# Optimization experiments

Hardware: AMD Instinct MI355X
Metric: run time of the kernel (lower is better)

Reference implementation:

```python
import jax, jax.numpy as jnp
import numpy as np

D = 256; DFFN = 1024; H = 8; NLVL = 4; NPNT = 4; HD = D // H
BS = 4; NQ = 100; NPTS = 25
SPATIAL = [(128, 128), (64, 64), (32, 32), (16, 16)]
LEN_IN = sum(h * w for h, w in SPATIAL)


def _ln(x, g, b, eps=1e-5):
    m = x.mean(-1, keepdims=True)
    v = ((x - m) ** 2).mean(-1, keepdims=True)
    return (x - m) * jax.lax.rsqrt(v + eps) * g + b


def _mha(q, k, v, w_in, b_in, w_out, b_out):
    # torch nn.MultiheadAttention math, batch-first layout [B,S,D]
    B, Sq, _ = q.shape; Sk = k.shape[1]
    wq, wk, wv = jnp.split(w_in, 3, 0); bq, bk, bv = jnp.split(b_in, 3)
    qh = (q @ wq.T + bq).reshape(B, Sq, H, HD).transpose(0, 2, 1, 3)
    kh = (k @ wk.T + bk).reshape(B, Sk, H, HD).transpose(0, 2, 1, 3)
    vh = (v @ wv.T + bv).reshape(B, Sk, H, HD).transpose(0, 2, 1, 3)
    a = jax.nn.softmax(jnp.einsum('bhqd,bhkd->bhqk', qh, kh) * (1.0 / float(np.sqrt(HD))), -1)
    o = jnp.einsum('bhqk,bhkd->bhqd', a, vh).transpose(0, 2, 1, 3).reshape(B, Sq, D)
    return o @ w_out.T + b_out


def _msdeform(query, ref, src, off_w, off_b, aw_w, aw_b, val_w, val_b, out_w, out_b):
    # MSDeformAttn: per-query multi-level bilinear sampling + weighted aggregation
    bs, Lq, _ = query.shape
    value = (src @ val_w.T + val_b).reshape(bs, LEN_IN, H, HD)
    off = (query @ off_w.T + off_b).reshape(bs, Lq, H, NLVL, NPNT, 2)
    aw = jax.nn.softmax((query @ aw_w.T + aw_b).reshape(bs, Lq, H, NLVL * NPNT), -1)
    aw = aw.reshape(bs, Lq, H, NLVL, NPNT)
    norm = jnp.array([[w, h] for h, w in SPATIAL], jnp.float32)  # (W,H) per level
    loc = ref[:, :, None, :, None, :] + off / norm[None, None, None, :, None, :]
    out = jnp.zeros((bs, H, Lq, HD), query.dtype)
    start = 0
    for l, (hh, ww) in enumerate(SPATIAL):
        v_l = value[:, start:start + hh * ww].transpose(0, 2, 1, 3)  # [bs,H,hw,HD]
        start += hh * ww
        # grid_sample align_corners=False pixel coords: loc*size - 0.5
        x = (loc[:, :, :, l, :, 0] * ww - 0.5).transpose(0, 2, 1, 3).reshape(bs, H, Lq * NPNT)
        y = (loc[:, :, :, l, :, 1] * hh - 0.5).transpose(0, 2, 1, 3).reshape(bs, H, Lq * NPNT)
        x0 = jnp.floor(x); y0 = jnp.floor(y); wx = x - x0; wy = y - y0
        x0i = x0.astype(jnp.int32); y0i = y0.astype(jnp.int32); x1i = x0i + 1; y1i = y0i + 1
        def g(xi, yi):
            valid = ((xi >= 0) & (xi < ww) & (yi >= 0) & (yi < hh)).astype(query.dtype)
            idx = jnp.clip(yi, 0, hh - 1) * ww + jnp.clip(xi, 0, ww - 1)
            return jnp.take_along_axis(v_l, idx[..., None], axis=2) * valid[..., None]
        s = (g(x0i, y0i) * ((1 - wx) * (1 - wy))[..., None]
             + g(x1i, y0i) * (wx * (1 - wy))[..., None]
             + g(x0i, y1i) * ((1 - wx) * wy)[..., None]
             + g(x1i, y1i) * (wx * wy)[..., None])
        s = s.reshape(bs, H, Lq, NPNT, HD)
        out = out + (s * aw[:, :, :, l].transpose(0, 2, 1, 3)[..., None]).sum(3)
    return out.transpose(0, 2, 1, 3).reshape(bs, Lq, D) @ out_w.T + out_b


def _fwd(tgt, query_pos, reference_points, src,
         w_in_intra, b_in_intra, w_out_intra, b_out_intra, g_norm_intra, b_norm_intra,
         w_in_inter, b_in_inter, w_out_inter, b_out_inter, g_norm_inter, b_norm_inter,
         off_w, off_b, aw_w, aw_b, val_w, val_b, co_w, co_b, g_norm_cross, b_norm_cross,
         lin1_w, lin1_b, lin2_w, lin2_b, g_norm3, b_norm3):
    bs, nq, npts, d = tgt.shape
    # intra-instance self-attention (over control points)
    q = (tgt + query_pos).reshape(bs * nq, npts, d)
    t2 = _mha(q, q, tgt.reshape(bs * nq, npts, d), w_in_intra, b_in_intra, w_out_intra, b_out_intra)
    tgt = _ln(tgt + t2.reshape(bs, nq, npts, d), g_norm_intra, b_norm_intra)
    # inter-instance self-attention (over queries), no pos embed per source code
    ti = tgt.transpose(0, 2, 1, 3).reshape(bs * npts, nq, d)
    t2 = _mha(ti, ti, ti, w_in_inter, b_in_inter, w_out_inter, b_out_inter)
    ti = _ln(ti + t2, g_norm_inter, b_norm_inter).reshape(bs, npts, nq, d).transpose(0, 2, 1, 3)
    # deformable cross-attention
    ref = jnp.broadcast_to(reference_points[:, :, None], (bs, nq, npts, NLVL, 2)).reshape(bs, nq * npts, NLVL, 2)
    qc = (ti + query_pos).reshape(bs, nq * npts, d)
    t2 = _msdeform(qc, ref, src, off_w, off_b, aw_w, aw_b, val_w, val_b, co_w, co_b).reshape(bs, nq, npts, d)
    tgt = _ln(ti + t2, g_norm_cross, b_norm_cross)
    # FFN
    ff = jax.nn.relu(tgt @ lin1_w.T + lin1_b) @ lin2_w.T + lin2_b
    return _ln(tgt + ff, g_norm3, b_norm3)


def setup_inputs() -> dict:
    key = jax.random.key(0)
    ki = iter(jax.random.split(key, 40))
    def rn(shape, sc=0.02):
        return jax.random.normal(next(ki), shape, jnp.float32) * sc
    inp = dict(
        tgt=jax.random.normal(next(ki), (BS, NQ, NPTS, D), jnp.float32),
        query_pos=jax.random.normal(next(ki), (BS, NQ, NPTS, D), jnp.float32),
        reference_points=jax.random.uniform(next(ki), (BS, NQ, NLVL, 2), jnp.float32),
        src=jax.random.normal(next(ki), (BS, LEN_IN, D), jnp.float32),
        w_in_intra=rn((3 * D, D)), b_in_intra=jnp.zeros((3 * D,), jnp.float32),
        w_out_intra=rn((D, D)), b_out_intra=jnp.zeros((D,), jnp.float32),
        g_norm_intra=jnp.ones((D,), jnp.float32), b_norm_intra=jnp.zeros((D,), jnp.float32),
        w_in_inter=rn((3 * D, D)), b_in_inter=jnp.zeros((3 * D,), jnp.float32),
        w_out_inter=rn((D, D)), b_out_inter=jnp.zeros((D,), jnp.float32),
        g_norm_inter=jnp.ones((D,), jnp.float32), b_norm_inter=jnp.zeros((D,), jnp.float32),
        off_w=rn((H * NLVL * NPNT * 2, D), 0.001), off_b=rn((H * NLVL * NPNT * 2,), 0.5),
        aw_w=rn((H * NLVL * NPNT, D)), aw_b=jnp.zeros((H * NLVL * NPNT,), jnp.float32),
        val_w=rn((D, D)), val_b=jnp.zeros((D,), jnp.float32),
        co_w=rn((D, D)), co_b=jnp.zeros((D,), jnp.float32),
        g_norm_cross=jnp.ones((D,), jnp.float32), b_norm_cross=jnp.zeros((D,), jnp.float32),
        lin1_w=rn((DFFN, D)), lin1_b=jnp.zeros((DFFN,), jnp.float32),
        lin2_w=rn((D, DFFN)), lin2_b=jnp.zeros((D,), jnp.float32),
        g_norm3=jnp.ones((D,), jnp.float32), b_norm3=jnp.zeros((D,), jnp.float32),
        src_spatial_shapes=jnp.array(SPATIAL, jnp.int32),
        level_start_index=jnp.array(np.cumsum([0] + [h * w for h, w in SPATIAL[:-1]]), jnp.int32),
    )
    return inp


def reference(tgt, query_pos, reference_points, src,
              w_in_intra, b_in_intra, w_out_intra, b_out_intra, g_norm_intra, b_norm_intra,
              w_in_inter, b_in_inter, w_out_inter, b_out_inter, g_norm_inter, b_norm_inter,
              off_w, off_b, aw_w, aw_b, val_w, val_b, co_w, co_b, g_norm_cross, b_norm_cross,
              lin1_w, lin1_b, lin2_w, lin2_b, g_norm3, b_norm3,
              src_spatial_shapes, level_start_index):
    # spatial shapes / level starts are compile-time constants (SPATIAL); args kept for signature parity
    return _fwd(tgt, query_pos, reference_points, src,
                w_in_intra, b_in_intra, w_out_intra, b_out_intra, g_norm_intra, b_norm_intra,
                w_in_inter, b_in_inter, w_out_inter, b_out_inter, g_norm_inter, b_norm_inter,
                off_w, off_b, aw_w, aw_b, val_w, val_b, co_w, co_b, g_norm_cross, b_norm_cross,
                lin1_w, lin1_b, lin2_w, lin2_b, g_norm3, b_norm3)
```

## Files before the change

### kernel.cpp

```cpp
#include <hip/hip_runtime.h>
#include <math.h>

#define DMODEL 256
#define HEADS  8
#define HDIM   32
#define BS     4
#define NQ     100
#define NPTS   25
#define LQ     2500
#define M10K   10000
#define LEN_IN 21760
#define MVAL   87040

typedef float f32x4 __attribute__((ext_vector_type(4)));
typedef short s16x8 __attribute__((ext_vector_type(8)));
typedef unsigned short u16;

static __device__ __forceinline__ short f2bf(float f) {
    unsigned u = __builtin_bit_cast(unsigned, f);
    u = (u + 0x7fffu + ((u >> 16) & 1u)) >> 16;
    return (short)u;
}
static __device__ __forceinline__ unsigned pack2(float lo, float hi) {
    return (unsigned)(u16)f2bf(lo) | ((unsigned)(u16)f2bf(hi) << 16);
}
static __device__ __forceinline__ float bf_lo(unsigned u) {
    return __builtin_bit_cast(float, u << 16);
}
static __device__ __forceinline__ float bf_hi(unsigned u) {
    return __builtin_bit_cast(float, u & 0xffff0000u);
}

#define LDSK   40
#define LDSK64 72

__global__ __launch_bounds__(256) void fat_stage0_kernel(
    const float* __restrict__ s0, const float* __restrict__ s1,
    const float* __restrict__ s2, const float* __restrict__ s3,
    const float* __restrict__ s4, const float* __restrict__ s5,
    const float* __restrict__ s6, const float* __restrict__ s7,
    const float* __restrict__ s8, const float* __restrict__ s9,
    u16* __restrict__ dst,
    const float* __restrict__ a, const float* __restrict__ b,
    u16* __restrict__ xb, u16* __restrict__ ab)
{
    if (blockIdx.x < 624) {
        int t8 = (blockIdx.x * 256 + threadIdx.x) * 8;
        if (t8 >= 1277952) return;
        const float* s; int base;
        if      (t8 <  196608) { s = s0; base = 0;       }
        else if (t8 <  262144) { s = s1; base = 196608;  }
        else if (t8 <  458752) { s = s2; base = 262144;  }
        else if (t8 <  524288) { s = s3; base = 458752;  }
        else if (t8 <  589824) { s = s4; base = 524288;  }
        else if (t8 <  622592) { s = s5; base = 589824;  }
        else if (t8 <  688128) { s = s6; base = 622592;  }
        else if (t8 <  753664) { s = s7; base = 688128;  }
        else if (t8 < 1015808) { s = s8; base = 753664;  }
        else                   { s = s9; base = 1015808; }
        const float* p = s + (t8 - base);
        float4 fa = *(const float4*)p;
        float4 fb = *(const float4*)(p + 4);
        s16x8 v;
        v[0]=f2bf(fa.x); v[1]=f2bf(fa.y); v[2]=f2bf(fa.z); v[3]=f2bf(fa.w);
        v[4]=f2bf(fb.x); v[5]=f2bf(fb.y); v[6]=f2bf(fb.z); v[7]=f2bf(fb.w);
        *(s16x8*)(dst + t8) = v;
    } else {
        int i = (blockIdx.x - 624) * 256 + threadIdx.x;
        size_t o = (size_t)i * 8;
        float4 a0 = *(const float4*)(a + o);
        float4 a1 = *(const float4*)(a + o + 4);
        s16x8 v;
        v[0]=f2bf(a0.x); v[1]=f2bf(a0.y); v[2]=f2bf(a0.z); v[3]=f2bf(a0.w);
        v[4]=f2bf(a1.x); v[5]=f2bf(a1.y); v[6]=f2bf(a1.z); v[7]=f2bf(a1.w);
        *(s16x8*)(ab + o) = v;
        float4 b0 = *(const float4*)(b + o);
        float4 b1 = *(const float4*)(b + o + 4);
        a0.x += b0.x; a0.y += b0.y; a0.z += b0.z; a0.w += b0.w;
        a1.x += b1.x; a1.y += b1.y; a1.z += b1.z; a1.w += b1.w;
        s16x8 w;
        w[0]=f2bf(a0.x); w[1]=f2bf(a0.y); w[2]=f2bf(a0.z); w[3]=f2bf(a0.w);
        w[4]=f2bf(a1.x); w[5]=f2bf(a1.y); w[6]=f2bf(a1.z); w[7]=f2bf(a1.w);
        *(s16x8*)(xb + o) = w;
    }
}


static __device__ __forceinline__ void body_value64(
    char* smem_, const float* __restrict__ A, const u16* __restrict__ W,
    const float* __restrict__ bias, u16* __restrict__ C, int bx, int by)
{
    short* As = (short*)smem_;
    short* Ws = (short*)(smem_ + 5120);

    const int tid = threadIdx.x;
    const int n0 = bx * 128;
    const int m0 = by * 64;

    const int arow = tid >> 2;
    const int ak = (tid & 3) * 8;
    const int wrow = tid >> 1;
    const int wk = (tid & 1) * 16;

    const float* aptr = A + (size_t)(m0 + arow) * 256 + ak;
    const u16* wptr = W + (size_t)(n0 + wrow) * 256 + wk;

    const int wave = tid >> 6;
    const int wm = wave & 1, wn = wave >> 1;
    const int lane = tid & 63;
    const int lrow = lane & 15, kq = lane >> 4;

    f32x4 acc[2][4];
#pragma unroll
    for (int i = 0; i < 2; ++i)
#pragma unroll
        for (int j = 0; j < 4; ++j) acc[i][j] = (f32x4)(0.f);

    float4 pa0 = *(const float4*)aptr;
    float4 pa1 = *(const float4*)(aptr + 4);
    s16x8 w0 = *(const s16x8*)wptr;
    s16x8 w1 = *(const s16x8*)(wptr + 8);

    for (int k0 = 0; k0 < 256; k0 += 32) {
        s16x8 av;
        av[0]=f2bf(pa0.x); av[1]=f2bf(pa0.y); av[2]=f2bf(pa0.z); av[3]=f2bf(pa0.w);
        av[4]=f2bf(pa1.x); av[5]=f2bf(pa1.y); av[6]=f2bf(pa1.z); av[7]=f2bf(pa1.w);
        *(s16x8*)&As[arow * LDSK + ak]     = av;
        *(s16x8*)&Ws[wrow * LDSK + wk]     = w0;
        *(s16x8*)&Ws[wrow * LDSK + wk + 8] = w1;
        __syncthreads();
        if (k0 + 32 < 256) {
            pa0 = *(const float4*)(aptr + k0 + 32);
            pa1 = *(const float4*)(aptr + k0 + 36);
            w0 = *(const s16x8*)(wptr + k0 + 32);
            w1 = *(const s16x8*)(wptr + k0 + 40);
        }

        s16x8 af[2], bfv[4];
#pragma unroll
        for (int i = 0; i < 2; ++i)
            af[i] = *(const s16x8*)&As[(wm * 32 + i * 16 + lrow) * LDSK + kq * 8];
#pragma unroll
        for (int j = 0; j < 4; ++j)
            bfv[j] = *(const s16x8*)&Ws[(wn * 64 + j * 16 + lrow) * LDSK + kq * 8];
#pragma unroll
        for (int i = 0; i < 2; ++i)
#pragma unroll
            for (int j = 0; j < 4; ++j)
                acc[i][j] = __builtin_amdgcn_mfma_f32_16x16x32_bf16(af[i], bfv[j], acc[i][j], 0, 0, 0);
        __syncthreads();
    }

#pragma unroll
    for (int i = 0; i < 2; ++i)
#pragma unroll
        for (int j = 0; j < 4; ++j) {
            int col = n0 + wn * 64 + j * 16 + lrow;
            float bv = bias[col];
#pragma unroll
            for (int reg = 0; reg < 4; ++reg) {
                int gmo = m0 + wm * 32 + i * 16 + kq * 4 + reg;
                C[(size_t)gmo * 256 + col] = (u16)f2bf(acc[i][j][reg] + bv);
            }
        }
}

static __device__ __forceinline__ void body_mfma128(
    char* smem_, const u16* __restrict__ A, const u16* __restrict__ W,
    const float* __restrict__ bias, u16* __restrict__ Cv, int bx, int by)
{
    short* As = (short*)smem_;
    short* Ws = (short*)(smem_ + 10240);

    const int tid = threadIdx.x;
    const int m0 = by * 128, n0 = bx * 128;
    const int srow = tid >> 1;
    const int sk = (tid & 1) * 16;
    const int wave = tid >> 6;
    const int wm = wave & 1, wn = wave >> 1;
    const int lane = tid & 63;
    const int lrow = lane & 15, kq = lane >> 4;

    const int gm = m0 + srow;
    const u16* aptr = A + (size_t)gm * 256 + sk;
    const u16* wptr = W + (size_t)(n0 + srow) * 256 + sk;

    f32x4 acc[4][4];
#pragma unroll
    for (int i = 0; i < 4; ++i)
#pragma unroll
        for (int j = 0; j < 4; ++j) acc[i][j] = (f32x4)(0.f);

    s16x8 a0 = (s16x8)0, a1 = (s16x8)0, w0, w1;
    if (gm < M10K) { a0 = *(const s16x8*)aptr; a1 = *(const s16x8*)(aptr + 8); }
    w0 = *(const s16x8*)wptr; w1 = *(const s16x8*)(wptr + 8);

    for (int k0 = 0; k0 < 256; k0 += 32) {
        *(s16x8*)&As[srow * LDSK + sk]     = a0;
        *(s16x8*)&As[srow * LDSK + sk + 8] = a1;
        *(s16x8*)&Ws[srow * LDSK + sk]     = w0;
        *(s16x8*)&Ws[srow * LDSK + sk + 8] = w1;
        __syncthreads();
        if (k0 + 32 < 256) {
            if (gm < M10K) {
                a0 = *(const s16x8*)(aptr + k0 + 32);
                a1 = *(const s16x8*)(aptr + k0 + 40);
            }
            w0 = *(const s16x8*)(wptr + k0 + 32);
            w1 = *(const s16x8*)(wptr + k0 + 40);
        }

        s16x8 af[4], bfv[4];
#pragma unroll
        for (int i = 0; i < 4; ++i)
            af[i] = *(const s16x8*)&As[(wm * 64 + i * 16 + lrow) * LDSK + kq * 8];
#pragma unroll
        for (int j = 0; j < 4; ++j)
            bfv[j] = *(const s16x8*)&Ws[(wn * 64 + j * 16 + lrow) * LDSK + kq * 8];
#pragma unroll
        for (int i = 0; i < 4; ++i)
#pragma unroll
            for (int j = 0; j < 4; ++j)
                acc[i][j] = __builtin_amdgcn_mfma_f32_16x16x32_bf16(af[i], bfv[j], acc[i][j], 0, 0, 0);
        __syncthreads();
    }

#pragma unroll
    for (int i = 0; i < 4; ++i)
#pragma unroll
        for (int j = 0; j < 4; ++j) {
            int col = n0 + wn * 64 + j * 16 + lrow;
            float bv = bias[col];
#pragma unroll
            for (int reg = 0; reg < 4; ++reg) {
                int gmo = m0 + wm * 64 + i * 16 + kq * 4 + reg;
                if (gmo < M10K)
                    Cv[(size_t)gmo * 768 + col] = (u16)f2bf(acc[i][j][reg] + bv);
            }
        }
}

static __device__ __forceinline__ void body_mfma64(
    char* smem_, const u16* __restrict__ A, const u16* __restrict__ W,
    const float* __restrict__ bias, u16* __restrict__ Cv, int bx, int by)
{
    short* As = (short*)smem_;
    short* Ws = (short*)(smem_ + 9216);

    const int tid = threadIdx.x;
    const int m0 = by * 64, n0 = bx * 64;
    const int srow = tid >> 2;
    const int sk = (tid & 3) * 16;
    const int wave = tid >> 6;
    const int wm = wave & 1, wn = wave >> 1;
    const int lane = tid & 63;
    const int lrow = lane & 15, kq = lane >> 4;

    const int gm = m0 + srow;
    const u16* aptr = A + (size_t)gm * 256 + sk;
    const u16* wptr = W + (size_t)(n0 + srow) * 256 + sk;

    f32x4 acc[2][2];
#pragma unroll
    for (int i = 0; i < 2; ++i)
#pragma unroll
        for (int j = 0; j < 2; ++j) acc[i][j] = (f32x4)(0.f);

    s16x8 a0 = (s16x8)0, a1 = (s16x8)0, w0, w1;
    if (gm < M10K) { a0 = *(const s16x8*)aptr; a1 = *(const s16x8*)(aptr + 8); }
    w0 = *(const s16x8*)wptr; w1 = *(const s16x8*)(wptr + 8);

    for (int k0 = 0; k0 < 256; k0 += 64) {
        *(s16x8*)&As[srow * LDSK64 + sk]     = a0;
        *(s16x8*)&As[srow * LDSK64 + sk + 8] = a1;
        *(s16x8*)&Ws[srow * LDSK64 + sk]     = w0;
        *(s16x8*)&Ws[srow * LDSK64 + sk + 8] = w1;
        __syncthreads();
        if (k0 + 64 < 256) {
            if (gm < M10K) {
                a0 = *(const s16x8*)(aptr + k0 + 64);
                a1 = *(const s16x8*)(aptr + k0 + 72);
            }
            w0 = *(const s16x8*)(wptr + k0 + 64);
            w1 = *(const s16x8*)(wptr + k0 + 72);
        }

#pragma unroll
        for (int s = 0; s < 2; ++s) {
            s16x8 af[2], bfv[2];
#pragma unroll
            for (int i = 0; i < 2; ++i)
                af[i] = *(const s16x8*)&As[(wm * 32 + i * 16 + lrow) * LDSK64 + s * 32 + kq * 8];
#pragma unroll
            for (int j = 0; j < 2; ++j)
                bfv[j] = *(const s16x8*)&Ws[(wn * 32 + j * 16 + lrow) * LDSK64 + s * 32 + kq * 8];
#pragma unroll
            for (int i = 0; i < 2; ++i)
#pragma unroll
                for (int j = 0; j < 2; ++j)
                    acc[i][j] = __builtin_amdgcn_mfma_f32_16x16x32_bf16(af[i], bfv[j], acc[i][j], 0, 0, 0);
        }
        __syncthreads();
    }

#pragma unroll
    for (int i = 0; i < 2; ++i)
#pragma unroll
        for (int j = 0; j < 2; ++j) {
            int col = n0 + wn * 32 + j * 16 + lrow;
            float bv = bias[col];
#pragma unroll
            for (int reg = 0; reg < 4; ++reg) {
                int gmo = m0 + wm * 32 + i * 16 + kq * 4 + reg;
                if (gmo < M10K)
                    Cv[(size_t)gmo * 768 + col] = (u16)f2bf(acc[i][j][reg] + bv);
            }
        }
}

__global__ __launch_bounds__(256) void fat_stage1_kernel(
    const float* __restrict__ src, const u16* __restrict__ wval,
    const float* __restrict__ valb, u16* __restrict__ valueb,
    const u16* __restrict__ x1b, const u16* __restrict__ wqk,
    const float* __restrict__ bqk, u16* __restrict__ qkvb,
    const u16* __restrict__ tgtb, const u16* __restrict__ wv,
    const float* __restrict__ bv, u16* __restrict__ qkvb_v)
{
    __shared__ __align__(16) char smem[20480];
    const int b = blockIdx.x;
    if (b < 2720) {
        body_value64(smem, src, wval, valb, valueb, b & 1, b >> 1);
    } else if (b < 3036) {
        const int bb = b - 2720;
        body_mfma128(smem, x1b, wqk, bqk, qkvb, bb & 3, bb >> 2);
    } else {
        const int bb = b - 3036;
        body_mfma64(smem, tgtb, wv, bv, qkvb_v, bb & 3, bb >> 2);
    }
}

__global__ __launch_bounds__(256) void gemm_mfma_kernel(
    const u16* __restrict__ A, int lda,
    const u16* __restrict__ W, int K,
    const float* __restrict__ bias,
    void* __restrict__ Cv, int ldc,
    int M, int relu, int out_bf16,
    int ncut, const float* __restrict__ bias2,
    float* __restrict__ Cv2, int ldc2)
{
    __shared__ short As[64 * LDSK64];
    __shared__ short Ws[64 * LDSK64];

    const int tid = threadIdx.x;
    const int m0 = blockIdx.y * 64, n0 = blockIdx.x * 64;
    const int srow = tid >> 2;
    const int sk = (tid & 3) * 16;
    const int wave = tid >> 6;
    const int wm = wave & 1, wn = wave >> 1;
    const int lane = tid & 63;
    const int lrow = lane & 15;
    const int kq = lane >> 4;

    const int gm = m0 + srow;
    const u16* aptr = A + (size_t)gm * lda + sk;
    const u16* wptr = W + (size_t)(n0 + srow) * K + sk;

    f32x4 acc[2][2];
#pragma unroll
    for (int i = 0; i < 2; ++i)
#pragma unroll
        for (int j = 0; j < 2; ++j) acc[i][j] = (f32x4)(0.f);

    s16x8 a0 = (s16x8)0, a1 = (s16x8)0, w0, w1;
    if (gm < M) { a0 = *(const s16x8*)aptr; a1 = *(const s16x8*)(aptr + 8); }
    w0 = *(const s16x8*)wptr; w1 = *(const s16x8*)(wptr + 8);

    for (int k0 = 0; k0 < K; k0 += 64) {
        *(s16x8*)&As[srow * LDSK64 + sk]     = a0;
        *(s16x8*)&As[srow * LDSK64 + sk + 8] = a1;
        *(s16x8*)&Ws[srow * LDSK64 + sk]     = w0;
        *(s16x8*)&Ws[srow * LDSK64 + sk + 8] = w1;
        __syncthreads();
        if (k0 + 64 < K) {
            if (gm < M) {
                a0 = *(const s16x8*)(aptr + k0 + 64);
                a1 = *(const s16x8*)(aptr + k0 + 72);
            }
            w0 = *(const s16x8*)(wptr + k0 + 64);
            w1 = *(const s16x8*)(wptr + k0 + 72);
        }

#pragma unroll
        for (int s = 0; s < 2; ++s) {
            s16x8 af[2], bfv[2];
#pragma unroll
            for (int i = 0; i < 2; ++i)
                af[i] = *(const s16x8*)&As[(wm * 32 + i * 16 + lrow) * LDSK64 + s * 32 + kq * 8];
#pragma unroll
            for (int j = 0; j < 2; ++j)
                bfv[j] = *(const s16x8*)&Ws[(wn * 32 + j * 16 + lrow) * LDSK64 + s * 32 + kq * 8];
#pragma unroll
            for (int i = 0; i < 2; ++i)
#pragma unroll
                for (int j = 0; j < 2; ++j)
                    acc[i][j] = __builtin_amdgcn_mfma_f32_16x16x32_bf16(af[i], bfv[j], acc[i][j], 0, 0, 0);
        }
        __syncthreads();
    }

#pragma unroll
    for (int i = 0; i < 2; ++i)
#pragma unroll
        for (int j = 0; j < 2; ++j) {
            int col = n0 + wn * 32 + j * 16 + lrow;
            float bv = (col < ncut) ? bias[col] : bias2[col - ncut];
#pragma unroll
            for (int reg = 0; reg < 4; ++reg) {
                int gmo = m0 + wm * 32 + i * 16 + kq * 4 + reg;
                if (gmo < M) {
                    float v = acc[i][j][reg] + bv;
                    if (relu) v = fmaxf(v, 0.f);
                    if (col < ncut) {
                        if (out_bf16)
                            ((u16*)Cv)[(size_t)gmo * ldc + col] = (u16)f2bf(v);
                        else
                            ((float*)Cv)[(size_t)gmo * ldc + col] = v;
                    } else {
                        Cv2[(size_t)gmo * ldc2 + (col - ncut)] = v;
                    }
                }
            }
        }
}

__global__ __launch_bounds__(256) void gemm_mfma128_kernel(
    const u16* __restrict__ A, int lda,
    const u16* __restrict__ W, int K,
    const float* __restrict__ bias,
    void* __restrict__ Cv, int ldc,
    int M, int relu, int out_bf16)
{
    __shared__ short As[128 * LDSK];
    __shared__ short Ws[128 * LDSK];

    const int tid = threadIdx.x;
    const int m0 = blockIdx.y * 128, n0 = blockIdx.x * 128;

    const int srow = tid >> 1;
    const int sk = (tid & 1) * 16;

    const int wave = tid >> 6;
    const int wm = wave & 1, wn = wave >> 1;
    const int lane = tid & 63;
    const int lrow = lane & 15;
    const int kq = lane >> 4;

    const int gm = m0 + srow;
    const u16* aptr = A + (size_t)gm * lda + sk;
    const u16* wptr = W + (size_t)(n0 + srow) * K + sk;

    f32x4 acc[4][4];
#pragma unroll
    for (int i = 0; i < 4; ++i)
#pragma unroll
        for (int j = 0; j < 4; ++j) acc[i][j] = (f32x4)(0.f);

    s16x8 a0 = (s16x8)0, a1 = (s16x8)0, w0, w1;
    if (gm < M) { a0 = *(const s16x8*)aptr; a1 = *(const s16x8*)(aptr + 8); }
    w0 = *(const s16x8*)wptr; w1 = *(const s16x8*)(wptr + 8);

    for (int k0 = 0; k0 < K; k0 += 32) {
        *(s16x8*)&As[srow * LDSK + sk]     = a0;
        *(s16x8*)&As[srow * LDSK + sk + 8] = a1;
        *(s16x8*)&Ws[srow * LDSK + sk]     = w0;
        *(s16x8*)&Ws[srow * LDSK + sk + 8] = w1;
        __syncthreads();
        if (k0 + 32 < K) {
            if (gm < M) {
                a0 = *(const s16x8*)(aptr + k0 + 32);
                a1 = *(const s16x8*)(aptr + k0 + 40);
            }
            w0 = *(const s16x8*)(wptr + k0 + 32);
            w1 = *(const s16x8*)(wptr + k0 + 40);
        }

        s16x8 af[4], bfv[4];
#pragma unroll
        for (int i = 0; i < 4; ++i)
            af[i] = *(const s16x8*)&As[(wm * 64 + i * 16 + lrow) * LDSK + kq * 8];
#pragma unroll
        for (int j = 0; j < 4; ++j)
            bfv[j] = *(const s16x8*)&Ws[(wn * 64 + j * 16 + lrow) * LDSK + kq * 8];
#pragma unroll
        for (int i = 0; i < 4; ++i)
#pragma unroll
            for (int j = 0; j < 4; ++j)
                acc[i][j] = __builtin_amdgcn_mfma_f32_16x16x32_bf16(af[i], bfv[j], acc[i][j], 0, 0, 0);
        __syncthreads();
    }

#pragma unroll
    for (int i = 0; i < 4; ++i)
#pragma unroll
        for (int j = 0; j < 4; ++j) {
            int col = n0 + wn * 64 + j * 16 + lrow;
            float bv = bias[col];
#pragma unroll
            for (int reg = 0; reg < 4; ++reg) {
                int gmo = m0 + wm * 64 + i * 16 + kq * 4 + reg;
                if (gmo < M) {
                    float v = acc[i][j][reg] + bv;
                    if (relu) v = fmaxf(v, 0.f);
                    if (out_bf16)
                        ((u16*)Cv)[(size_t)gmo * ldc + col] = (u16)f2bf(v);
                    else
                        ((float*)Cv)[(size_t)gmo * ldc + col] = v;
                }
            }
        }
}

__global__ __launch_bounds__(256) void inter_attn_mfma_kernel(
    const u16* __restrict__ qkv, u16* __restrict__ out, float scale)
{
    __shared__ __align__(16) u16 Qs[112 * 40];
    __shared__ __align__(16) u16 Ks[112 * 40];
    __shared__ __align__(16) u16 Vt[32 * 136];
    __shared__ __align__(16) u16 Ps[112 * 136];

    const int b = blockIdx.x, h = blockIdx.y;
    const u16* base = qkv + (size_t)b * 100 * 768;
    const int tid = threadIdx.x;
    const int wave = tid >> 6, lane = tid & 63;
    const int lr = lane & 15, quad = lane >> 4;

    for (int i = tid; i < 12 * 20; i += 256) {
        int row = 100 + i / 20, c = (i % 20) * 2;
        *(unsigned*)&Qs[row * 40 + c] = 0;
        *(unsigned*)&Ks[row * 40 + c] = 0;
    }
    for (int i = tid; i < 2176; i += 256) ((unsigned*)Vt)[i] = 0;
    for (int i = tid; i < 7616; i += 256) ((unsigned*)Ps)[i] = 0;
    __syncthreads();

    for (int idx = tid; idx < 2400; idx += 256) {
        int row = idx / 24, s = idx % 24;
        const u16* p = (s < 8)  ? base + row * 768 + h * 32 + s * 4
                     : (s < 16) ? base + row * 768 + 256 + h * 32 + (s - 8) * 4
                                : base + row * 768 + 512 + h * 32 + (s - 16) * 4;
        if (s < 8) {
            *(uint2*)&Qs[row * 40 + s * 4] = *(const uint2*)p;
        } else if (s < 16) {
            *(uint2*)&Ks[row * 40 + (s - 8) * 4] = *(const uint2*)p;
        } else {
            int d0 = (s - 16) * 4;
            Vt[(d0 + 0) * 136 + row] = p[0];
            Vt[(d0 + 1) * 136 + row] = p[1];
            Vt[(d0 + 2) * 136 + row] = p[2];
            Vt[(d0 + 3) * 136 + row] = p[3];
        }
    }
    __syncthreads();

#pragma unroll 1
    for (int rr = 0; rr < 2; ++rr) {
        int rt = wave + rr * 4;
        if (rt < 7) {
            s16x8 aq = *(const s16x8*)&Qs[(rt * 16 + lr) * 40 + quad * 8];
            f32x4 sc[7];
#pragma unroll
            for (int ct = 0; ct < 7; ++ct) {
                s16x8 bk = *(const s16x8*)&Ks[(ct * 16 + lr) * 40 + quad * 8];
                sc[ct] = __builtin_amdgcn_mfma_f32_16x16x32_bf16(aq, bk, (f32x4)(0.f), 0, 0, 0);
            }
            const bool colok[7] = {true, true, true, true, true, true, (lr < 4)};
#pragma unroll
            for (int reg = 0; reg < 4; ++reg) {
                float mx = -1e30f;
#pragma unroll
                for (int ct = 0; ct < 7; ++ct) {
                    float sv = sc[ct][reg] * scale;
                    sc[ct][reg] = sv;
                    if (colok[ct]) mx = fmaxf(mx, sv);
                }
#pragma unroll
                for (int d = 1; d < 16; d <<= 1) mx = fmaxf(mx, __shfl_xor(mx, d));
                float ssum = 0.f;
#pragma unroll
                for (int ct = 0; ct < 7; ++ct) {
                    float pv = colok[ct] ? __expf(sc[ct][reg] - mx) : 0.f;
                    sc[ct][reg] = pv;
                    ssum += pv;
                }
#pragma unroll
                for (int d = 1; d < 16; d <<= 1) ssum += __shfl_xor(ssum, d);
                float inv = 1.f / ssum;
                int prow = rt * 16 + quad * 4 + reg;
#pragma unroll
                for (int ct = 0; ct < 7; ++ct)
                    Ps[prow * 136 + ct * 16 + lr] = (u16)f2bf(sc[ct][reg] * inv);
            }
        }
    }
    __syncthreads();

#pragma unroll 1
    for (int rr = 0; rr < 2; ++rr) {
        int rt = wave + rr * 4;
        if (rt < 7) {
            f32x4 o0 = (f32x4)(0.f), o1 = (f32x4)(0.f);
#pragma unroll
            for (int kk = 0; kk < 4; ++kk) {
                s16x8 ap = *(const s16x8*)&Ps[(rt * 16 + lr) * 136 + kk * 32 + quad * 8];
                s16x8 bv0 = *(const s16x8*)&Vt[lr * 136 + kk * 32 + quad * 8];
                s16x8 bv1 = *(const s16x8*)&Vt[(16 + lr) * 136 + kk * 32 + quad * 8];
                o0 = __builtin_amdgcn_mfma_f32_16x16x32_bf16(ap, bv0, o0, 0, 0, 0);
                o1 = __builtin_amdgcn_mfma_f32_16x16x32_bf16(ap, bv1, o1, 0, 0, 0);
            }
#pragma unroll
            for (int reg = 0; reg < 4; ++reg) {
                int q = rt * 16 + quad * 4 + reg;
                if (q < 100) {
                    u16* op = out + ((size_t)b * 100 + q) * 256 + h * 32;
                    op[lr]      = (u16)f2bf(o0[reg]);
                    op[16 + lr] = (u16)f2bf(o1[reg]);
                }
            }
        }
    }
}

__global__ __launch_bounds__(256) void intra_attn_kernel(
    const u16* __restrict__ qkv, u16* __restrict__ out, float scale)
{
    __shared__ float4 KV[25][128];

    const int b = blockIdx.x;
    const int h = threadIdx.x >> 5, r = threadIdx.x & 31;
    const u16* base = qkv + (size_t)b * 25 * 768;

    for (int idx = threadIdx.x; idx < 3200; idx += 256) {
        int row = idx >> 7, c = idx & 127;
        uint2 u = *(const uint2*)(base + row * 768 + 256 + c * 4);
        KV[row][c] = make_float4(bf_lo(u.x), bf_hi(u.x), bf_lo(u.y), bf_hi(u.y));
    }

    float q[32];
    if (r < 25) {
        const u16* qp = base + r * 768 + h * 32;
#pragma unroll
        for (int c4 = 0; c4 < 8; ++c4) {
            uint2 u = *(const uint2*)(qp + c4 * 4);
            q[c4*4+0] = bf_lo(u.x); q[c4*4+1] = bf_hi(u.x);
            q[c4*4+2] = bf_lo(u.y); q[c4*4+3] = bf_hi(u.y);
        }
    }
    __syncthreads();

    if (r < 25) {
        float m = -1e30f, l = 0.f, acc[32];
#pragma unroll
        for (int c = 0; c < 32; ++c) acc[c] = 0.f;
#pragma unroll 2
        for (int j = 0; j < 25; ++j) {
            const float4* kr = &KV[j][h * 8];
            float dot = 0.f;
#pragma unroll
            for (int c4 = 0; c4 < 8; ++c4) {
                float4 kf = kr[c4];
                dot = fmaf(q[c4*4+0], kf.x, dot);
                dot = fmaf(q[c4*4+1], kf.y, dot);
                dot = fmaf(q[c4*4+2], kf.z, dot);
                dot = fmaf(q[c4*4+3], kf.w, dot);
            }
            dot *= scale;
            float mn = fmaxf(m, dot);
            float alpha = __expf(m - mn);
            float p = __expf(dot - mn);
            l = l * alpha + p;
            const float4* vr = &KV[j][64 + h * 8];
#pragma unroll
            for (int c4 = 0; c4 < 8; ++c4) {
                float4 vf = vr[c4];
                acc[c4*4+0] = acc[c4*4+0] * alpha + p * vf.x;
                acc[c4*4+1] = acc[c4*4+1] * alpha + p * vf.y;
                acc[c4*4+2] = acc[c4*4+2] * alpha + p * vf.z;
                acc[c4*4+3] = acc[c4*4+3] * alpha + p * vf.w;
            }
            m = mn;
        }
        float inv = 1.f / l;
        unsigned* op = (unsigned*)(out + ((size_t)b * 25 + r) * 256 + h * 32);
#pragma unroll
        for (int c = 0; c < 16; ++c)
            op[c] = pack2(acc[2*c] * inv, acc[2*c+1] * inv);
    }
}

__global__ __launch_bounds__(256) void add_ln_kernel(
    const float* __restrict__ a, const float* __restrict__ b,
    const float* __restrict__ g, const float* __restrict__ beta,
    float* __restrict__ out, u16* __restrict__ out_bf,
    const float* __restrict__ qp, u16* __restrict__ qout,
    int transpose_mode)
{
    const int r = blockIdx.x * 4 + (threadIdx.x >> 6);
    const int lane = threadIdx.x & 63;
    const size_t co = (size_t)r * 256 + lane * 4;

    const float4 av = *(const float4*)(a + co);
    const float4 bv = *(const float4*)(b + co);
    float4 x;
    x.x = av.x + bv.x; x.y = av.y + bv.y; x.z = av.z + bv.z; x.w = av.w + bv.w;

    float s = x.x + x.y + x.z + x.w;
#pragma unroll
    for (int off = 32; off >= 1; off >>= 1) s += __shfl_xor(s, off);
    float mean = s * (1.f / 256.f);

    float dx = x.x - mean, dy = x.y - mean, dz = x.z - mean, dw = x.w - mean;
    float vs = dx * dx + dy * dy + dz * dz + dw * dw;
#pragma unroll
    for (int off = 32; off >= 1; off >>= 1) vs += __shfl_xor(vs, off);
    float rstd = rsqrtf(vs * (1.f / 256.f) + 1e-5f);

    size_t ro = r;
    if (transpose_mode == 1) {
        int q = r % 100; int bp = r / 100; int p = bp % 25; int bb = bp / 25;
        ro = ((size_t)bb * 100 + q) * 25 + p;
    } else if (transpose_mode == 2) {
        int p = r % 25; int t = r / 25; int q = t % 100; int bb = t / 100;
        ro = ((size_t)bb * 25 + p) * 100 + q;
    }
    const size_t oo = ro * 256 + lane * 4;

    const float4 gv = *(const float4*)(g + lane * 4);
    const float4 bt = *(const float4*)(beta + lane * 4);
    float4 y;
    y.x = dx * rstd * gv.x + bt.x;
    y.y = dy * rstd * gv.y + bt.y;
    y.z = dz * rstd * gv.z + bt.z;
    y.w = dw * rstd * gv.w + bt.w;

    *(float4*)(out + oo) = y;
    if (out_bf) {
        uint2 pk = make_uint2(pack2(y.x, y.y), pack2(y.z, y.w));
        *(uint2*)(out_bf + oo) = pk;
    }
    if (qout) {
        const float4 qv = *(const float4*)(qp + oo);
        uint2 pk = make_uint2(pack2(y.x + qv.x, y.y + qv.y),
                              pack2(y.z + qv.z, y.w + qv.w));
        *(uint2*)(qout + oo) = pk;
    }
}

__global__ __launch_bounds__(256, 4) void msdeform_sample_kernel(
    const u16* __restrict__ value,
    const float* __restrict__ off,
    const float* __restrict__ awl,
    const float* __restrict__ refp,
    u16* __restrict__ sampled)
{
    const int unit = blockIdx.x * 8 + (threadIdx.x >> 5);
    const int t = threadIdx.x & 31;
    const int h = t >> 2, c8 = t & 3;
    const int b = unit / LQ, lq = unit - b * LQ;
    const int q = lq / NPTS;

    const float* awp = awl + (size_t)unit * 128 + h * 16;
    float w[16];
    float mx = -1e30f;
#pragma unroll
    for (int k = 0; k < 16; ++k) { w[k] = awp[k]; mx = fmaxf(mx, w[k]); }
    float sum = 0.f;
#pragma unroll
    for (int k = 0; k < 16; ++k) { w[k] = __expf(w[k] - mx); sum += w[k]; }
    const float inv = 1.f / sum;

    const float* offp = off + (size_t)unit * 256 + h * 32;
    const float* rp = refp + ((size_t)b * 100 + q) * 8;
    const u16* vbase = value + (size_t)b * LEN_IN * 256 + h * 32 + c8 * 8;

    float acc[8];
#pragma unroll
    for (int k = 0; k < 8; ++k) acc[k] = 0.f;

    int start = 0;
    const int sz[4] = {128, 64, 32, 16};
#pragma unroll
    for (int l = 0; l < 4; ++l) {
        const int hh = sz[l], ww = sz[l];
        const float rx = rp[l * 2 + 0], ry = rp[l * 2 + 1];
#pragma unroll 1
        for (int pt = 0; pt < 4; ++pt) {
            float ox = offp[(l * 4 + pt) * 2 + 0];
            float oy = offp[(l * 4 + pt) * 2 + 1];
            float x = rx * ww + ox - 0.5f;
            float y = ry * hh + oy - 0.5f;
            float x0f = floorf(x), y0f = floorf(y);
            float wx = x - x0f, wy = y - y0f;
            int x0 = (int)x0f, y0 = (int)y0f;
            int x1 = x0 + 1, y1 = y0 + 1;
            float aw = w[l * 4 + pt] * inv;

            int x0c = min(max(x0, 0), ww - 1), x1c = min(max(x1, 0), ww - 1);
            int y0c = min(max(y0, 0), hh - 1), y1c = min(max(y1, 0), hh - 1);
            float w00 = aw * (1.f - wx) * (1.f - wy);
            float w10 = aw * wx * (1.f - wy);
            float w01 = aw * (1.f - wx) * wy;
            float w11 = aw * wx * wy;
            if (!(x0 >= 0 && x0 < ww)) { w00 = 0.f; w01 = 0.f; }
            if (!(x1 >= 0 && x1 < ww)) { w10 = 0.f; w11 = 0.f; }
            if (!(y0 >= 0 && y0 < hh)) { w00 = 0.f; w10 = 0.f; }
            if (!(y1 >= 0 && y1 < hh)) { w01 = 0.f; w11 = 0.f; }

            uint4 u00 = *(const uint4*)(vbase + (size_t)(start + y0c * ww + x0c) * 256);
            uint4 u10 = *(const uint4*)(vbase + (size_t)(start + y0c * ww + x1c) * 256);
            uint4 u01 = *(const uint4*)(vbase + (size_t)(start + y1c * ww + x0c) * 256);
            uint4 u11 = *(const uint4*)(vbase + (size_t)(start + y1c * ww + x1c) * 256);

#define ACC4(u, wgt) \
            acc[0] = fmaf(wgt, bf_lo(u.x), acc[0]); \
            acc[1] = fmaf(wgt, bf_hi(u.x), acc[1]); \
            acc[2] = fmaf(wgt, bf_lo(u.y), acc[2]); \
            acc[3] = fmaf(wgt, bf_hi(u.y), acc[3]); \
            acc[4] = fmaf(wgt, bf_lo(u.z), acc[4]); \
            acc[5] = fmaf(wgt, bf_hi(u.z), acc[5]); \
            acc[6] = fmaf(wgt, bf_lo(u.w), acc[6]); \
            acc[7] = fmaf(wgt, bf_hi(u.w), acc[7]);
            ACC4(u00, w00); ACC4(u10, w10); ACC4(u01, w01); ACC4(u11, w11);
#undef ACC4
        }
        start += hh * ww;
    }

    uint4 pk;
    pk.x = pack2(acc[0], acc[1]); pk.y = pack2(acc[2], acc[3]);
    pk.z = pack2(acc[4], acc[5]); pk.w = pack2(acc[6], acc[7]);
    *(uint4*)(sampled + (size_t)unit * 256 + h * 32 + c8 * 8) = pk;
}

extern "C" void kernel_launch(void* const* d_in, const int* in_sizes, int n_in,
                              void* d_out, int out_size, void* d_ws, size_t ws_size,
                              hipStream_t stream)
{
    (void)in_sizes; (void)n_in; (void)out_size; (void)ws_size;

    const float* tgt        = (const float*)d_in[0];
    const float* query_pos  = (const float*)d_in[1];
    const float* refp       = (const float*)d_in[2];
    const float* src        = (const float*)d_in[3];
    const float* w_in_intra = (const float*)d_in[4];
    const float* b_in_intra = (const float*)d_in[5];
    const float* w_out_intra= (const float*)d_in[6];
    const float* b_out_intra= (const float*)d_in[7];
    const float* g_ln_intra = (const float*)d_in[8];
    const float* b_ln_intra = (const float*)d_in[9];
    const float* w_in_inter = (const float*)d_in[10];
    const float* b_in_inter = (const float*)d_in[11];
    const float* w_out_inter= (const float*)d_in[12];
    const float* b_out_inter= (const float*)d_in[13];
    const float* g_ln_inter = (const float*)d_in[14];
    const float* b_ln_inter = (const float*)d_in[15];
    const float* off_w      = (const float*)d_in[16];
    const float* off_b      = (const float*)d_in[17];
    const float* aw_w       = (const float*)d_in[18];
    const float* aw_b       = (const float*)d_in[19];
    const float* val_w      = (const float*)d_in[20];
    const float* val_b      = (const float*)d_in[21];
    const float* co_w       = (const float*)d_in[22];
    const float* co_b       = (const float*)d_in[23];
    const float* g_ln_cross = (const float*)d_in[24];
    const float* b_ln_cross = (const float*)d_in[25];
    const float* lin1_w     = (const float*)d_in[26];
    const float* lin1_b     = (const float*)d_in[27];
    const float* lin2_w     = (const float*)d_in[28];
    const float* lin2_b     = (const float*)d_in[29];
    const float* g_ln3      = (const float*)d_in[30];
    const float* b_ln3      = (const float*)d_in[31];

    float* ws    = (float*)d_ws;
    float* qkv   = ws;
    float* tmp   = ws + 7680000;
    u16*   attnb = (u16*)(ws + 10240000);
    float* tgt1  = ws + 11520000;
    float* ti    = ws + 14080000;
    u16*   tib   = (u16*)(ws + 16640000);
    float* tA    = ws + 17920000;
    u16*   qcb   = (u16*)(ws + 20480000);
    u16*   x1b   = (u16*)(ws + 21760000);
    u16*   tgtb  = (u16*)(ws + 23040000);
    float* awl   = ws + 24320000;
    u16*   valueb= (u16*)(ws + 25600000);
    u16*   wb    = (u16*)(ws + 36741120);
    float* out   = (float*)d_out;

    u16* qkvb = (u16*)qkv;

    u16* wb_in_intra  = wb;
    u16* wb_out_intra = wb + 196608;
    u16* wb_in_inter  = wb + 262144;
    u16* wb_out_inter = wb + 458752;
    u16* wb_off       = wb + 524288;
    u16* wb_val       = wb + 622592;
    u16* wb_co        = wb + 688128;
    u16* wb_lin1      = wb + 753664;
    u16* wb_lin2      = wb + 1015808;

    const float scale = 0.17677669529663687f;
    const int MB64  = (M10K + 63) / 64;
    const int MB128 = (M10K + 127) / 128;
    const int NC_OFF = 1 << 30;

    fat_stage0_kernel<<<1874, 256, 0, stream>>>(
        w_in_intra, w_out_intra, w_in_inter, w_out_inter, off_w,
        aw_w, val_w, co_w, lin1_w, lin2_w, wb,
        tgt, query_pos, x1b, tgtb);

    fat_stage1_kernel<<<3664, 256, 0, stream>>>(
        src, wb_val, val_b, valueb,
        x1b, wb_in_intra, b_in_intra, qkvb,
        tgtb, wb_in_intra + 512 * 256, b_in_intra + 512, qkvb + 512);

    intra_attn_kernel<<<400, 256, 0, stream>>>(qkvb, attnb, scale);
    gemm_mfma_kernel<<<dim3(4, MB64), 256, 0, stream>>>(attnb, 256, wb_out_intra, 256,
                                                        b_out_intra, tmp, 256, M10K, 0, 0,
                                                        NC_OFF, b_out_intra, (float*)0, 0);
    add_ln_kernel<<<2500, 256, 0, stream>>>(tgt, tmp, g_ln_intra, b_ln_intra,
                                            ti, tib, (const float*)0, (u16*)0, 2);

    gemm_mfma128_kernel<<<dim3(6, MB128), 256, 0, stream>>>(tib, 256, wb_in_inter, 256,
                                                            b_in_inter, qkvb, 768, M10K, 0, 1);
    inter_attn_mfma_kernel<<<dim3(100, 8), 256, 0, stream>>>(qkvb, attnb, scale);
    gemm_mfma_kernel<<<dim3(4, MB64), 256, 0, stream>>>(attnb, 256, wb_out_inter, 256,
                                                        b_out_inter, tmp, 256, M10K, 0, 0,
                                                        NC_OFF, b_out_inter, (float*)0, 0);
    add_ln_kernel<<<2500, 256, 0, stream>>>(ti, tmp, g_ln_inter, b_ln_inter,
                                            tA, (u16*)0, query_pos, qcb, 1);

    gemm_mfma_kernel<<<dim3(6, MB64), 256, 0, stream>>>(qcb, 256, wb_off, 256,
                                                        off_b, tgt1, 256, M10K, 0, 0,
                                                        256, aw_b, awl, 128);
    msdeform_sample_kernel<<<1250, 256, 0, stream>>>(valueb, tgt1, awl, refp, attnb);
    gemm_mfma_kernel<<<dim3(4, MB64), 256, 0, stream>>>(attnb, 256, wb_co, 256,
                                                        co_b, tmp, 256, M10K, 0, 0,
                                                        NC_OFF, co_b, (float*)0, 0);
    add_ln_kernel<<<2500, 256, 0, stream>>>(tA, tmp, g_ln_cross, b_ln_cross,
                                            ti, tib, (const float*)0, (u16*)0, 0);

    gemm_mfma128_kernel<<<dim3(8, MB128), 256, 0, stream>>>(tib, 256, wb_lin1, 256,
                                                            lin1_b, valueb, 1024, M10K, 1, 1);
    gemm_mfma_kernel<<<dim3(4, MB64), 256, 0, stream>>>(valueb, 1024, wb_lin2, 1024,
                                                        lin2_b, tmp, 256, M10K, 0, 0,
                                                        NC_OFF, lin2_b, (float*)0, 0);
    add_ln_kernel<<<2500, 256, 0, stream>>>(ti, tmp, g_ln3, b_ln3,
                                            out, (u16*)0, (const float*)0, (u16*)0, 0);
}
```

Measured before the change: 457.6 us.

## Fuse intra attention, output projection, residual add and LayerNorm into one kernel

Merges the intra-instance attention, its output projection GEMM (MFMA), the bias and residual add, and the LayerNorm with a transposed store into a single kernel with one block per instance. The attention output stays in LDS instead of round-tripping through global memory, and two kernel launches go away. K/V are now held as packed bf16 in LDS rather than expanded to float. Each block reloads the full 256x256 output weight, so weight traffic is replicated across 400 blocks. The sampling loop's unroll is also raised from 1 to 2.

```diff
diff --git a/kernel.cpp b/kernel.cpp
--- a/kernel.cpp
+++ b/kernel.cpp
@@ -630,19 +630,31 @@
     }
 }
 
-__global__ __launch_bounds__(256) void intra_attn_kernel(
-    const u16* __restrict__ qkv, u16* __restrict__ out, float scale)
-{
-    __shared__ float4 KV[25][128];
-
-    const int b = blockIdx.x;
-    const int h = threadIdx.x >> 5, r = threadIdx.x & 31;
-    const u16* base = qkv + (size_t)b * 25 * 768;
-
-    for (int idx = threadIdx.x; idx < 3200; idx += 256) {
+__global__ __launch_bounds__(256) void intra_fused_kernel(
+    const u16* __restrict__ qkv,
+    const u16* __restrict__ W,
+    const float* __restrict__ bias,
+    const float* __restrict__ res,
+    const float* __restrict__ g, const float* __restrict__ beta,
+    float* __restrict__ outf, u16* __restrict__ outbf,
+    float scale)
+{
+    __shared__ __align__(16) uint2 KVh[25][128];
+    __shared__ __align__(16) u16 Ao[32 * 264];
+    __shared__ short Ws[256 * LDSK];
+    __shared__ float redS[4][32];
+    __shared__ float redV[4][32];
+
+    const int inst = blockIdx.x;
+    const int tid = threadIdx.x;
+    const int h = tid >> 5, r = tid & 31;
+    const u16* base = qkv + (size_t)inst * 25 * 768;
+
+    for (int i = tid; i < 7 * 132; i += 256)
+        ((unsigned*)&Ao[25 * 264])[i] = 0;
+    for (int idx = tid; idx < 3200; idx += 256) {
         int row = idx >> 7, c = idx & 127;
-        uint2 u = *(const uint2*)(base + row * 768 + 256 + c * 4);
-        KV[row][c] = make_float4(bf_lo(u.x), bf_hi(u.x), bf_lo(u.y), bf_hi(u.y));
+        KVh[row][c] = *(const uint2*)(base + row * 768 + 256 + c * 4);
     }
 
     float q[32];
@@ -663,38 +675,138 @@
         for (int c = 0; c < 32; ++c) acc[c] = 0.f;
 #pragma unroll 2
         for (int j = 0; j < 25; ++j) {
-            const float4* kr = &KV[j][h * 8];
+            const uint2* kr = &KVh[j][h * 8];
             float dot = 0.f;
 #pragma unroll
             for (int c4 = 0; c4 < 8; ++c4) {
-                float4 kf = kr[c4];
-                dot = fmaf(q[c4*4+0], kf.x, dot);
-                dot = fmaf(q[c4*4+1], kf.y, dot);
-                dot = fmaf(q[c4*4+2], kf.z, dot);
-                dot = fmaf(q[c4*4+3], kf.w, dot);
+                uint2 u = kr[c4];
+                dot = fmaf(q[c4*4+0], bf_lo(u.x), dot);
+                dot = fmaf(q[c4*4+1], bf_hi(u.x), dot);
+                dot = fmaf(q[c4*4+2], bf_lo(u.y), dot);
+                dot = fmaf(q[c4*4+3], bf_hi(u.y), dot);
             }
             dot *= scale;
             float mn = fmaxf(m, dot);
             float alpha = __expf(m - mn);
             float p = __expf(dot - mn);
             l = l * alpha + p;
-            const float4* vr = &KV[j][64 + h * 8];
+            const uint2* vr = &KVh[j][64 + h * 8];
 #pragma unroll
             for (int c4 = 0; c4 < 8; ++c4) {
-                float4 vf = vr[c4];
-                acc[c4*4+0] = acc[c4*4+0] * alpha + p * vf.x;
-                acc[c4*4+1] = acc[c4*4+1] * alpha + p * vf.y;
-                acc[c4*4+2] = acc[c4*4+2] * alpha + p * vf.z;
-                acc[c4*4+3] = acc[c4*4+3] * alpha + p * vf.w;
+                uint2 u = vr[c4];
+                acc[c4*4+0] = acc[c4*4+0] * alpha + p * bf_lo(u.x);
+                acc[c4*4+1] = acc[c4*4+1] * alpha + p * bf_hi(u.x);
+                acc[c4*4+2] = acc[c4*4+2] * alpha + p * bf_lo(u.y);
+                acc[c4*4+3] = acc[c4*4+3] * alpha + p * bf_hi(u.y);
             }
             m = mn;
         }
         float inv = 1.f / l;
-        unsigned* op = (unsigned*)(out + ((size_t)b * 25 + r) * 256 + h * 32);
+        unsigned* op = (unsigned*)&Ao[r * 264 + h * 32];
 #pragma unroll
         for (int c = 0; c < 16; ++c)
             op[c] = pack2(acc[2*c] * inv, acc[2*c+1] * inv);
     }
+
+    const int wave = tid >> 6, lane = tid & 63;
+    const int lrow = lane & 15, kq = lane >> 4;
+
+    f32x4 acc2[2][4];
+#pragma unroll
+    for (int i = 0; i < 2; ++i)
+#pragma unroll
+        for (int j = 0; j < 4; ++j) acc2[i][j] = (f32x4)(0.f);
+
+    const u16* wptr = W + (size_t)tid * 256;
+    for (int k0 = 0; k0 < 256; k0 += 32) {
+        __syncthreads();
+        *(s16x8*)&Ws[tid * LDSK +  0] = *(const s16x8*)(wptr + k0);
+        *(s16x8*)&Ws[tid * LDSK +  8] = *(const s16x8*)(wptr + k0 + 8);
+        *(s16x8*)&Ws[tid * LDSK + 16] = *(const s16x8*)(wptr + k0 + 16);
+        *(s16x8*)&Ws[tid * LDSK + 24] = *(const s16x8*)(wptr + k0 + 24);
+        __syncthreads();
+
+        s16x8 af[2], bfv[4];
+#pragma unroll
+        for (int i = 0; i < 2; ++i)
+            af[i] = *(const s16x8*)&Ao[(i * 16 + lrow) * 264 + k0 + kq * 8];
+#pragma unroll
+        for (int j = 0; j < 4; ++j)
+            bfv[j] = *(const s16x8*)&Ws[(wave * 64 + j * 16 + lrow) * LDSK + kq * 8];
+#pragma unroll
+        for (int i = 0; i < 2; ++i)
+#pragma unroll
+            for (int j = 0; j < 4; ++j)
+                acc2[i][j] = __builtin_amdgcn_mfma_f32_16x16x32_bf16(af[i], bfv[j], acc2[i][j], 0, 0, 0);
+    }
+
+    const int qq = inst % 100, bb = inst / 100;
+    float x[2][4][4];
+#pragma unroll
+    for (int i = 0; i < 2; ++i)
+#pragma unroll
+        for (int j = 0; j < 4; ++j) {
+            const int col = wave * 64 + j * 16 + lrow;
+            const float bv = bias[col];
+#pragma unroll
+            for (int reg = 0; reg < 4; ++reg) {
+                const int rowp = i * 16 + kq * 4 + reg;
+                float rv = (rowp < 25) ? res[((size_t)inst * 25 + rowp) * 256 + col] : 0.f;
+                x[i][j][reg] = rv + (acc2[i][j][reg] + bv);
+            }
+        }
+
+#pragma unroll
+    for (int i = 0; i < 2; ++i)
+#pragma unroll
+        for (int reg = 0; reg < 4; ++reg) {
+            float s = x[i][0][reg] + x[i][1][reg] + x[i][2][reg] + x[i][3][reg];
+            s += __shfl_xor(s, 1); s += __shfl_xor(s, 2);
+            s += __shfl_xor(s, 4); s += __shfl_xor(s, 8);
+            if (lrow == 0) redS[wave][i * 16 + kq * 4 + reg] = s;
+        }
+    __syncthreads();
+    float mean[2][4];
+#pragma unroll
+    for (int i = 0; i < 2; ++i)
+#pragma unroll
+        for (int reg = 0; reg < 4; ++reg) {
+            const int rowp = i * 16 + kq * 4 + reg;
+            mean[i][reg] = (redS[0][rowp] + redS[1][rowp] + redS[2][rowp] + redS[3][rowp]) * (1.f / 256.f);
+        }
+#pragma unroll
+    for (int i = 0; i < 2; ++i)
+#pragma unroll
+        for (int reg = 0; reg < 4; ++reg) {
+            float vs = 0.f;
+#pragma unroll
+            for (int j = 0; j < 4; ++j) {
+                float d = x[i][j][reg] - mean[i][reg];
+                vs += d * d;
+            }
+            vs += __shfl_xor(vs, 1); vs += __shfl_xor(vs, 2);
+            vs += __shfl_xor(vs, 4); vs += __shfl_xor(vs, 8);
+            if (lrow == 0) redV[wave][i * 16 + kq * 4 + reg] = vs;
+        }
+    __syncthreads();
+
+#pragma unroll
+    for (int i = 0; i < 2; ++i)
+#pragma unroll
+        for (int reg = 0; reg < 4; ++reg) {
+            const int rowp = i * 16 + kq * 4 + reg;
+            if (rowp >= 25) continue;
+            const float rstd = rsqrtf(
+                (redV[0][rowp] + redV[1][rowp] + redV[2][rowp] + redV[3][rowp]) * (1.f / 256.f) + 1e-5f);
+            const size_t ro = ((size_t)bb * 25 + rowp) * 100 + qq;
+#pragma unroll
+            for (int j = 0; j < 4; ++j) {
+                const int col = wave * 64 + j * 16 + lrow;
+                const float y = (x[i][j][reg] - mean[i][reg]) * rstd * g[col] + beta[col];
+                outf[ro * 256 + col] = y;
+                outbf[ro * 256 + col] = (u16)f2bf(y);
+            }
+        }
 }
 
 __global__ __launch_bounds__(256) void add_ln_kernel(
@@ -792,7 +904,7 @@
     for (int l = 0; l < 4; ++l) {
         const int hh = sz[l], ww = sz[l];
         const float rx = rp[l * 2 + 0], ry = rp[l * 2 + 1];
-#pragma unroll 1
+#pragma unroll 2
         for (int pt = 0; pt < 4; ++pt) {
             float ox = offp[(l * 4 + pt) * 2 + 0];
             float oy = offp[(l * 4 + pt) * 2 + 1];
@@ -923,12 +1035,9 @@
         x1b, wb_in_intra, b_in_intra, qkvb,
         tgtb, wb_in_intra + 512 * 256, b_in_intra + 512, qkvb + 512);
 
-    intra_attn_kernel<<<400, 256, 0, stream>>>(qkvb, attnb, scale);
-    gemm_mfma_kernel<<<dim3(4, MB64), 256, 0, stream>>>(attnb, 256, wb_out_intra, 256,
-                                                        b_out_intra, tmp, 256, M10K, 0, 0,
-                                                        NC_OFF, b_out_intra, (float*)0, 0);
-    add_ln_kernel<<<2500, 256, 0, stream>>>(tgt, tmp, g_ln_intra, b_ln_intra,
-                                            ti, tib, (const float*)0, (u16*)0, 2);
+    intra_fused_kernel<<<400, 256, 0, stream>>>(qkvb, wb_out_intra, b_out_intra,
+                                                tgt, g_ln_intra, b_ln_intra,
+                                                ti, tib, scale);
 
     gemm_mfma128_kernel<<<dim3(6, MB128), 256, 0, stream>>>(tib, 256, wb_in_inter, 256,
                                                             b_in_inter, qkvb, 768, M10K, 0, 1);
```

Measured after the change: 456.1 us. Within noise of the previous version (-0.3%).
